# Performance work log

Measured on AMD Instinct MI355X. Metric: run time of the kernel, lower is better.

## Reference

```python
import jax, jax.numpy as jnp
import numpy as np

DIM = 2048
N_HEADS = 32
N_KV_HEADS = 8
HEAD_DIM = DIM // N_HEADS  # 64
N_REP = N_HEADS // N_KV_HEADS  # 4
B, S = 1, 2048


def _rope(t, cos, sin):
    # t: (b, s, h, head_dim); cos/sin: (s, head_dim//2)
    tr = t.reshape(*t.shape[:-1], -1, 2)
    a, b = tr[..., 0], tr[..., 1]
    c = cos[None, :, None, :]
    s_ = sin[None, :, None, :]
    ra = a * c - b * s_
    rb = a * s_ + b * c
    return jnp.stack([ra, rb], axis=-1).reshape(t.shape)


def setup_inputs() -> dict:
    key = jax.random.key(0)
    ks = jax.random.split(key, 6)
    sc = 1.0 / np.sqrt(DIM)
    x = jax.random.normal(ks[0], (B, S, DIM), dtype=jnp.float32)
    wq = jax.random.normal(ks[1], (DIM, N_HEADS * HEAD_DIM), dtype=jnp.float32) * sc
    wk = jax.random.normal(ks[2], (DIM, N_KV_HEADS * HEAD_DIM), dtype=jnp.float32) * sc
    wv = jax.random.normal(ks[3], (DIM, N_KV_HEADS * HEAD_DIM), dtype=jnp.float32) * sc
    wo = jax.random.normal(ks[4], (N_HEADS * HEAD_DIM, DIM), dtype=jnp.float32) * sc
    # rotary frequencies (theta = 500000 as in Llama3)
    inv = 1.0 / (500000.0 ** (np.arange(0, HEAD_DIM, 2, dtype=np.float32) / HEAD_DIM))
    ang = np.arange(S, dtype=np.float32)[:, None] * inv[None, :]
    freqs_cos = jnp.asarray(np.cos(ang), dtype=jnp.float32)
    freqs_sin = jnp.asarray(np.sin(ang), dtype=jnp.float32)
    # causal additive mask
    mask = jnp.triu(jnp.full((S, S), -1e9, dtype=jnp.float32), k=1)
    return {"x": x, "wq": wq, "wk": wk, "wv": wv, "wo": wo,
            "freqs_cos": freqs_cos, "freqs_sin": freqs_sin, "mask": mask,
            "start_pos": 0}


def reference(x, wq, wk, wv, wo, freqs_cos, freqs_sin, mask, start_pos):
    b, s, _ = x.shape
    xq = (x @ wq).reshape(b, s, N_HEADS, HEAD_DIM)
    xk = (x @ wk).reshape(b, s, N_KV_HEADS, HEAD_DIM)
    xv = (x @ wv).reshape(b, s, N_KV_HEADS, HEAD_DIM)
    xq = _rope(xq, freqs_cos, freqs_sin)
    xk = _rope(xk, freqs_cos, freqs_sin)
    # GQA without repeat_interleave: view queries as (b, s, kv, rep, d)
    q = xq.reshape(b, s, N_KV_HEADS, N_REP, HEAD_DIM)
    scale = 1.0 / np.sqrt(HEAD_DIM)
    # scores: (b, kv, rep, q, k)
    scores = jnp.einsum('bqkrd,bskd->bkrqs', q, xk) * scale
    scores = scores + mask[None, None, None, :, :]
    probs = jax.nn.softmax(scores.astype(jnp.float32), axis=-1).astype(x.dtype)
    out = jnp.einsum('bkrqs,bskd->bqkrd', probs, xv)
    out = out.reshape(b, s, N_HEADS * HEAD_DIM)
    return out @ wo
```

## Files before the change

### kernel.cpp

```cpp
#include <hip/hip_runtime.h>
#include <hip/hip_bf16.h>

#define DIM 2048
#define S_LEN 2048
#define N_HEADS 32
#define N_KV_HEADS 8
#define HEAD_DIM 64
#define KV_DIM (N_KV_HEADS * HEAD_DIM)
#define QKV_N (DIM + 2 * KV_DIM)
#define QSCALE 0.18033688011112042f

typedef __attribute__((ext_vector_type(8))) short bf16x8;
typedef __attribute__((ext_vector_type(4))) float f32x4;

__device__ __forceinline__ unsigned short bf16_of(float f) {
    __hip_bfloat16 h = __float2bfloat16(f);
    return *reinterpret_cast<unsigned short*>(&h);
}
__device__ __forceinline__ float f_of_bf16(unsigned short u) {
    unsigned int x = ((unsigned int)u) << 16;
    return __uint_as_float(x);
}
__device__ __forceinline__ void gl_lds16(const void* g, void* l) {
    __builtin_amdgcn_global_load_lds((const __attribute__((address_space(1))) void*)g,
                                     (__attribute__((address_space(3))) void*)l, 16, 0, 0);
}
__device__ __forceinline__ unsigned int pack2tr(float lo, float hi) {
    return __builtin_amdgcn_perm(__float_as_uint(hi), __float_as_uint(lo), 0x07060302u);
}

__global__ __launch_bounds__(256) void prep(const float* __restrict__ x,
                                            const float* __restrict__ wq,
                                            const float* __restrict__ wk,
                                            const float* __restrict__ wv,
                                            const float* __restrict__ wo,
                                            unsigned short* __restrict__ xbf,
                                            unsigned short* __restrict__ wqkvT,
                                            unsigned short* __restrict__ woT) {
    __shared__ float tile[64][65];
    const int t = threadIdx.x;
    int b = blockIdx.x;
    if (b < 4096) {
        int idx = b * 256 + t;
        float4 f = ((const float4*)x)[idx];
        ushort4 u;
        u.x = bf16_of(f.x); u.y = bf16_of(f.y); u.z = bf16_of(f.z); u.w = bf16_of(f.w);
        ((ushort4*)xbf)[idx] = u;
        return;
    }
    b -= 4096;
    const float* src;
    unsigned short* dst;
    int src_cols, bx, by;
    if (b < 1024)      { src = wq; dst = wqkvT;                                src_cols = DIM;    bx = b & 31;          by = b >> 5; }
    else if (b < 1280) { src = wk; dst = wqkvT + (size_t)DIM * DIM;            src_cols = KV_DIM; bx = (b - 1024) & 7;  by = (b - 1024) >> 3; }
    else if (b < 1536) { src = wv; dst = wqkvT + (size_t)(DIM + KV_DIM) * DIM; src_cols = KV_DIM; bx = (b - 1280) & 7;  by = (b - 1280) >> 3; }
    else               { src = wo; dst = woT;                                  src_cols = DIM;    bx = (b - 1536) & 31; by = (b - 1536) >> 5; }
    const int c0 = bx * 64, r0 = by * 64;
#pragma unroll
    for (int i = 0; i < 16; i++) {
        int idx = t + i * 256;
        int r = idx >> 6, c = idx & 63;
        tile[r][c] = src[(size_t)(r0 + r) * src_cols + c0 + c];
    }
    __syncthreads();
#pragma unroll
    for (int i = 0; i < 16; i++) {
        int idx = t + i * 256;
        int r = idx >> 6, c = idx & 63;
        dst[(size_t)(c0 + r) * DIM + r0 + c] = bf16_of(tile[c][r]);
    }
}

__global__ __launch_bounds__(256) void gemm_bt64(const unsigned short* __restrict__ A,
                                                 const unsigned short* __restrict__ Bt,
                                                 void* __restrict__ Cv,
                                                 int M, int N, int K, int c_bf16) {
    __shared__ unsigned short As[128 * 64];
    __shared__ unsigned short Bs[64 * 64];
    const int tid = threadIdx.x;
    const int wave = tid >> 6, lane = tid & 63;
    const int m16 = lane & 15, quad = lane >> 4;
    const int m0 = blockIdx.y * 128, n0 = blockIdx.x * 64;
    const int wm = (wave >> 1) * 64, wn = (wave & 1) * 32;

    const int lrow = lane >> 3;
    const int gc = (lane & 7) ^ lrow;
    const unsigned short* Ab = A + (size_t)(m0 + wave * 8 + lrow) * K + gc * 8;
    const unsigned short* Bb = Bt + (size_t)(n0 + wave * 8 + lrow) * K + gc * 8;

    f32x4 acc[4][2];
#pragma unroll
    for (int mb = 0; mb < 4; mb++)
#pragma unroll
        for (int nb = 0; nb < 2; nb++) acc[mb][nb] = (f32x4){0.f, 0.f, 0.f, 0.f};

    for (int k0 = 0; k0 < K; k0 += 64) {
#pragma unroll
        for (int g = 0; g < 4; g++)
            gl_lds16(Ab + (size_t)g * 32 * K + k0, &As[(g * 32 + wave * 8) * 64]);
#pragma unroll
        for (int g = 0; g < 2; g++)
            gl_lds16(Bb + (size_t)g * 32 * K + k0, &Bs[(g * 32 + wave * 8) * 64]);
        __syncthreads();
#pragma unroll
        for (int ks = 0; ks < 2; ks++) {
            const int ch = (ks * 4 + quad) ^ (m16 & 7);
            bf16x8 af[4], bfr[2];
#pragma unroll
            for (int mb = 0; mb < 4; mb++)
                af[mb] = *(const bf16x8*)&As[(wm + mb * 16 + m16) * 64 + ch * 8];
#pragma unroll
            for (int nb = 0; nb < 2; nb++)
                bfr[nb] = *(const bf16x8*)&Bs[(wn + nb * 16 + m16) * 64 + ch * 8];
#pragma unroll
            for (int mb = 0; mb < 4; mb++)
#pragma unroll
                for (int nb = 0; nb < 2; nb++)
                    acc[mb][nb] = __builtin_amdgcn_mfma_f32_16x16x32_bf16(af[mb], bfr[nb], acc[mb][nb], 0, 0, 0);
        }
        __syncthreads();
    }

    if (c_bf16) {
        unsigned short* C = (unsigned short*)Cv;
#pragma unroll
        for (int mb = 0; mb < 4; mb++)
#pragma unroll
            for (int nb = 0; nb < 2; nb++)
#pragma unroll
                for (int r = 0; r < 4; r++)
                    C[(size_t)(m0 + wm + mb * 16 + quad * 4 + r) * N + n0 + wn + nb * 16 + m16] =
                        bf16_of(acc[mb][nb][r]);
    } else {
        float* C = (float*)Cv;
#pragma unroll
        for (int mb = 0; mb < 4; mb++)
#pragma unroll
            for (int nb = 0; nb < 2; nb++)
#pragma unroll
                for (int r = 0; r < 4; r++)
                    C[(size_t)(m0 + wm + mb * 16 + quad * 4 + r) * N + n0 + wn + nb * 16 + m16] =
                        acc[mb][nb][r];
    }
}

__global__ __launch_bounds__(256) void rope_tv(const unsigned short* __restrict__ qkv,
                                               unsigned short* __restrict__ qbf,
                                               unsigned short* __restrict__ kbf,
                                               unsigned short* __restrict__ vbt,
                                               const float* __restrict__ fcos,
                                               const float* __restrict__ fsin) {
    __shared__ unsigned short tile[64][65];
    const int t = threadIdx.x;
    int b = blockIdx.x;
    if (b < 2560) {
        int idx = b * 256 + t;
        const int nq = S_LEN * N_HEADS * 8;
        int s, j, srcoff, dstoff;
        unsigned short* dst;
        float osc;
        if (idx < nq) {
            s = idx >> 8;
            int rem = idx & 255;
            int h = rem >> 3;
            j = rem & 7;
            srcoff = s * QKV_N + h * 64 + j * 8;
            dstoff = s * DIM + h * 64 + j * 8;
            dst = qbf;
            osc = QSCALE;
        } else {
            int t2 = idx - nq;
            s = t2 >> 6;
            int rem = t2 & 63;
            int h = rem >> 3;
            j = rem & 7;
            srcoff = s * QKV_N + DIM + h * 64 + j * 8;
            dstoff = s * KV_DIM + h * 64 + j * 8;
            dst = kbf;
            osc = 1.0f;
        }
        bf16x8 v8 = *(const bf16x8*)&qkv[srcoff];
        float4 c4 = *(const float4*)&fcos[s * 32 + j * 4];
        float4 s4 = *(const float4*)&fsin[s * 32 + j * 4];
        float cs[4] = {c4.x, c4.y, c4.z, c4.w};
        float sn[4] = {s4.x, s4.y, s4.z, s4.w};
        bf16x8 o;
#pragma unroll
        for (int p = 0; p < 4; p++) {
            float a = f_of_bf16((unsigned short)v8[2 * p]);
            float bb = f_of_bf16((unsigned short)v8[2 * p + 1]);
            o[2 * p]     = (short)bf16_of((a * cs[p] - bb * sn[p]) * osc);
            o[2 * p + 1] = (short)bf16_of((a * sn[p] + bb * cs[p]) * osc);
        }
        *(bf16x8*)&dst[dstoff] = o;
        return;
    }
    b -= 2560;
    const int d0 = (b & 7) * 64;
    const int s0 = (b >> 3) * 64;
#pragma unroll
    for (int i = 0; i < 16; i++) {
        int idx = t + i * 256;
        int r = idx >> 6, c = idx & 63;
        tile[r][c] = qkv[(size_t)(s0 + r) * QKV_N + DIM + KV_DIM + d0 + c];
    }
    __syncthreads();
#pragma unroll
    for (int i = 0; i < 16; i++) {
        int idx = t + i * 256;
        int r = idx >> 6, c = idx & 63;
        int key = s0 + c;
        int kl = key & 127;
        int kp = (kl & 0x60) | ((kl & 0x0C) << 1) | ((kl & 0x10) >> 2) | (kl & 3);
        vbt[(size_t)(d0 + r) * S_LEN + (key & ~127) + kp] = tile[c][r];
    }
}

__global__ __launch_bounds__(256) void attn_mfma5(const unsigned short* __restrict__ qb,
                                                  const unsigned short* __restrict__ kb,
                                                  const unsigned short* __restrict__ vbt,
                                                  unsigned short* __restrict__ out) {
    const int h  = blockIdx.y;
    const int bx = blockIdx.x;
    const int kh = h >> 2;
    const int tid  = threadIdx.x;
    const int wave = tid >> 6;
    const int lane = tid & 63;
    const int m16  = lane & 15;
    const int quad = lane >> 4;

    __shared__ unsigned short Ks[2][128 * 64];
    __shared__ unsigned short Vt[2][64 * 128];

    const int lrow8 = lane >> 3;
    const int kc    = (lane & 7) ^ lrow8;
    const int lrow4 = lane >> 4;
    const int vc    = (lane & 15) ^ ((wave * 4 + lrow4) & 7);

    const unsigned short* Kbase = kb + (size_t)kh * 64 + (size_t)(wave * 8 + lrow8) * KV_DIM + kc * 8;
    const unsigned short* Vbase = vbt + (size_t)(kh * 64 + wave * 4 + lrow4) * S_LEN + vc * 8;

    bf16x8 ones;
#pragma unroll
    for (int i = 0; i < 8; i++) ones[i] = (short)0x3F80;

#pragma unroll
    for (int half = 0; half < 2; half++) {
        const int qt = half ? bx : (31 - bx);
        const int q0 = qt * 64;
        const int n_iter = (qt >> 1) + 1;

        bf16x8 qa[2];
        {
            const int qrow = q0 + wave * 16 + m16;
#pragma unroll
            for (int ks = 0; ks < 2; ks++)
                qa[ks] = *(const bf16x8*)&qb[(size_t)qrow * DIM + h * 64 + ks * 32 + quad * 8];
        }

        f32x4 o_acc[4];
#pragma unroll
        for (int nb = 0; nb < 4; nb++) o_acc[nb] = (f32x4){0.f, 0.f, 0.f, 0.f};
        f32x4 l_acc = (f32x4){0.f, 0.f, 0.f, 0.f};
        float m_s = -1e30f;
        const int qrow_lane = q0 + wave * 16 + m16;
        const int orow_base = q0 + wave * 16 + quad * 4;

        if (half) __syncthreads();

#pragma unroll
        for (int g = 0; g < 4; g++) {
            gl_lds16(Kbase + (size_t)(g * 32) * KV_DIM, &Ks[0][(g * 32 + wave * 8) * 64]);
            gl_lds16(Vbase + (size_t)g * 16 * S_LEN, &Vt[0][(g * 16 + wave * 4) * 128]);
        }

        for (int kt = 0; kt < n_iter; kt++) {
            __syncthreads();
            if (kt + 1 < n_iter) {
                const int nb2 = (kt + 1) & 1;
#pragma unroll
                for (int g = 0; g < 4; g++) {
                    gl_lds16(Kbase + (size_t)((kt + 1) * 128 + g * 32) * KV_DIM,
                             &Ks[nb2][(g * 32 + wave * 8) * 64]);
                    gl_lds16(Vbase + (size_t)g * 16 * S_LEN + (kt + 1) * 128,
                             &Vt[nb2][(g * 16 + wave * 4) * 128]);
                }
            }
            const unsigned short* K_ = Ks[kt & 1];
            const unsigned short* V_ = Vt[kt & 1];

            f32x4 sc[8];
#pragma unroll
            for (int cb = 0; cb < 8; cb++) sc[cb] = (f32x4){0.f, 0.f, 0.f, 0.f};
#pragma unroll
            for (int ks = 0; ks < 2; ks++) {
                const int slot = (ks * 4 + quad) ^ (m16 & 7);
#pragma unroll
                for (int cb = 0; cb < 8; cb++) {
                    bf16x8 kf = *(const bf16x8*)&K_[(cb * 16 + m16) * 64 + slot * 8];
                    sc[cb] = __builtin_amdgcn_mfma_f32_16x16x32_bf16(kf, qa[ks], sc[cb], 0, 0, 0);
                }
            }

            if (kt == n_iter - 1) {
#pragma unroll
                for (int cb = 0; cb < 8; cb++) {
                    int key = kt * 128 + cb * 16 + quad * 4;
#pragma unroll
                    for (int r = 0; r < 4; r++)
                        if (key + r > qrow_lane) sc[cb][r] = -1e30f;
                }
            }

            float rmax = fmaxf(fmaxf(sc[0][0], sc[0][1]), fmaxf(sc[0][2], sc[0][3]));
#pragma unroll
            for (int cb = 1; cb < 8; cb++) {
                float c1 = fmaxf(fmaxf(sc[cb][0], sc[cb][1]), fmaxf(sc[cb][2], sc[cb][3]));
                rmax = fmaxf(rmax, c1);
            }
            rmax = fmaxf(rmax, __shfl_xor(rmax, 16, 64));
            rmax = fmaxf(rmax, __shfl_xor(rmax, 32, 64));

            float mnew = fmaxf(m_s, rmax);
            float alpha = __builtin_amdgcn_exp2f(m_s - mnew);
            m_s = mnew;

#pragma unroll
            for (int cb = 0; cb < 8; cb++)
#pragma unroll
                for (int r = 0; r < 4; r++)
                    sc[cb][r] = __builtin_amdgcn_exp2f(sc[cb][r] - mnew);

            unsigned int P01[8], P23[8];
#pragma unroll
            for (int cb = 0; cb < 8; cb++) {
                P01[cb] = pack2tr(sc[cb][0], sc[cb][1]);
                P23[cb] = pack2tr(sc[cb][2], sc[cb][3]);
            }

#pragma unroll
            for (int r = 0; r < 4; r++) {
                float a_r = __shfl(alpha, quad * 4 + r, 64);
#pragma unroll
                for (int nb = 0; nb < 4; nb++) o_acc[nb][r] *= a_r;
                l_acc[r] *= a_r;
            }

#pragma unroll
            for (int ks = 0; ks < 4; ks++) {
                union { unsigned int u[4]; bf16x8 v; } pa;
                pa.u[0] = P01[2 * ks];     pa.u[1] = P23[2 * ks];
                pa.u[2] = P01[2 * ks + 1]; pa.u[3] = P23[2 * ks + 1];
                const int slot = (ks * 4 + quad) ^ (m16 & 7);
#pragma unroll
                for (int nb = 0; nb < 4; nb++) {
                    bf16x8 vf = *(const bf16x8*)&V_[(nb * 16 + m16) * 128 + slot * 8];
                    o_acc[nb] = __builtin_amdgcn_mfma_f32_16x16x32_bf16(pa.v, vf, o_acc[nb], 0, 0, 0);
                }
                l_acc = __builtin_amdgcn_mfma_f32_16x16x32_bf16(pa.v, ones, l_acc, 0, 0, 0);
            }
        }

#pragma unroll
        for (int r = 0; r < 4; r++) {
            float inv_l = 1.f / l_acc[r];
#pragma unroll
            for (int nb = 0; nb < 4; nb++)
                out[(size_t)(orow_base + r) * DIM + h * 64 + nb * 16 + m16] =
                    bf16_of(o_acc[nb][r] * inv_l);
        }
    }
}

extern "C" void kernel_launch(void* const* d_in, const int* in_sizes, int n_in,
                              void* d_out, int out_size, void* d_ws, size_t ws_size,
                              hipStream_t stream) {
    const float* x    = (const float*)d_in[0];
    const float* wq   = (const float*)d_in[1];
    const float* wk   = (const float*)d_in[2];
    const float* wv   = (const float*)d_in[3];
    const float* wo   = (const float*)d_in[4];
    const float* fcos = (const float*)d_in[5];
    const float* fsin = (const float*)d_in[6];

    char* ws = (char*)d_ws;
    const size_t MB = 1024 * 1024;
    unsigned short* xbf    = (unsigned short*)(ws);
    unsigned short* wqkvT  = (unsigned short*)(ws + 8 * MB);
    unsigned short* woT    = (unsigned short*)(ws + 20 * MB);
    unsigned short* qkvbf  = (unsigned short*)(ws + 28 * MB);
    unsigned short* vbt    = (unsigned short*)(ws + 40 * MB);
    unsigned short* qbf    = (unsigned short*)(ws + 8 * MB);
    unsigned short* kbf    = (unsigned short*)(ws + 16 * MB);
    unsigned short* attnbf = (unsigned short*)(ws);

    prep<<<4096 + 2560, 256, 0, stream>>>(x, wq, wk, wv, wo, xbf, wqkvT, woT);

    gemm_bt64<<<dim3(QKV_N / 64, S_LEN / 128), 256, 0, stream>>>(xbf, wqkvT, qkvbf,
                                                                 S_LEN, QKV_N, DIM, 1);

    rope_tv<<<2560 + 256, 256, 0, stream>>>(qkvbf, qbf, kbf, vbt, fcos, fsin);

    attn_mfma5<<<dim3(16, N_HEADS), 256, 0, stream>>>(qbf, kbf, vbt, attnbf);

    gemm_bt64<<<dim3(DIM / 64, S_LEN / 128), 256, 0, stream>>>(attnbf, woT, d_out,
                                                               S_LEN, DIM, DIM, 0);
}
```

Before: 228.3 us.

## Widen QKV GEMM tile, add lazy softmax rescale, setprio and max3 in attention

The QKV projection now uses a new 128x128-tile GEMM kernel, so each block covers twice the N width and gets more operand reuse per LDS load. In the attention kernel, the online-softmax rescale of the accumulators is skipped unless the running max grows by more than 8 (log2 units), the row-max reduction uses v_max3, and the MFMA sections are wrapped in s_setprio. The prep transpose now writes two bf16 values per store. The lazy rescale lets exponentials grow up to 2^8 before rescaling, which costs a little numerical headroom, and the larger GEMM tile launches half as many blocks.

```diff
diff --git a/kernel.cpp b/kernel.cpp
--- a/kernel.cpp
+++ b/kernel.cpp
@@ -27,6 +27,11 @@
 }
 __device__ __forceinline__ unsigned int pack2tr(float lo, float hi) {
     return __builtin_amdgcn_perm(__float_as_uint(hi), __float_as_uint(lo), 0x07060302u);
+}
+__device__ __forceinline__ float max3f(float a, float b, float c) {
+    float d;
+    asm("v_max3_f32 %0, %1, %2, %3" : "=v"(d) : "v"(a), "v"(b), "v"(c));
+    return d;
 }
 
 __global__ __launch_bounds__(256) void prep(const float* __restrict__ x,
@@ -65,10 +70,13 @@
     }
     __syncthreads();
 #pragma unroll
-    for (int i = 0; i < 16; i++) {
+    for (int i = 0; i < 8; i++) {
         int idx = t + i * 256;
-        int r = idx >> 6, c = idx & 63;
-        dst[(size_t)(c0 + r) * DIM + r0 + c] = bf16_of(tile[c][r]);
+        int rr = idx >> 5, cc = (idx & 31) * 2;
+        ushort2 u2;
+        u2.x = bf16_of(tile[cc][rr]);
+        u2.y = bf16_of(tile[cc + 1][rr]);
+        *(ushort2*)&dst[(size_t)(c0 + rr) * DIM + r0 + cc] = u2;
     }
 }
 
@@ -138,6 +146,78 @@
         for (int mb = 0; mb < 4; mb++)
 #pragma unroll
             for (int nb = 0; nb < 2; nb++)
+#pragma unroll
+                for (int r = 0; r < 4; r++)
+                    C[(size_t)(m0 + wm + mb * 16 + quad * 4 + r) * N + n0 + wn + nb * 16 + m16] =
+                        acc[mb][nb][r];
+    }
+}
+
+__global__ __launch_bounds__(256) void gemm_bt128(const unsigned short* __restrict__ A,
+                                                  const unsigned short* __restrict__ Bt,
+                                                  void* __restrict__ Cv,
+                                                  int M, int N, int K, int c_bf16) {
+    __shared__ unsigned short As[128 * 64];
+    __shared__ unsigned short Bs[128 * 64];
+    const int tid = threadIdx.x;
+    const int wave = tid >> 6, lane = tid & 63;
+    const int m16 = lane & 15, quad = lane >> 4;
+    const int m0 = blockIdx.y * 128, n0 = blockIdx.x * 128;
+    const int wm = (wave >> 1) * 64, wn = (wave & 1) * 64;
+
+    const int lrow = lane >> 3;
+    const int gc = (lane & 7) ^ lrow;
+    const unsigned short* Ab = A + (size_t)(m0 + wave * 8 + lrow) * K + gc * 8;
+    const unsigned short* Bb = Bt + (size_t)(n0 + wave * 8 + lrow) * K + gc * 8;
+
+    f32x4 acc[4][4];
+#pragma unroll
+    for (int mb = 0; mb < 4; mb++)
+#pragma unroll
+        for (int nb = 0; nb < 4; nb++) acc[mb][nb] = (f32x4){0.f, 0.f, 0.f, 0.f};
+
+    for (int k0 = 0; k0 < K; k0 += 64) {
+#pragma unroll
+        for (int g = 0; g < 4; g++) {
+            gl_lds16(Ab + (size_t)g * 32 * K + k0, &As[(g * 32 + wave * 8) * 64]);
+            gl_lds16(Bb + (size_t)g * 32 * K + k0, &Bs[(g * 32 + wave * 8) * 64]);
+        }
+        __syncthreads();
+#pragma unroll
+        for (int ks = 0; ks < 2; ks++) {
+            const int ch = (ks * 4 + quad) ^ (m16 & 7);
+            bf16x8 af[4], bfr[4];
+#pragma unroll
+            for (int mb = 0; mb < 4; mb++)
+                af[mb] = *(const bf16x8*)&As[(wm + mb * 16 + m16) * 64 + ch * 8];
+#pragma unroll
+            for (int nb = 0; nb < 4; nb++)
+                bfr[nb] = *(const bf16x8*)&Bs[(wn + nb * 16 + m16) * 64 + ch * 8];
+#pragma unroll
+            for (int mb = 0; mb < 4; mb++)
+#pragma unroll
+                for (int nb = 0; nb < 4; nb++)
+                    acc[mb][nb] = __builtin_amdgcn_mfma_f32_16x16x32_bf16(af[mb], bfr[nb], acc[mb][nb], 0, 0, 0);
+        }
+        __syncthreads();
+    }
+
+    if (c_bf16) {
+        unsigned short* C = (unsigned short*)Cv;
+#pragma unroll
+        for (int mb = 0; mb < 4; mb++)
+#pragma unroll
+            for (int nb = 0; nb < 4; nb++)
+#pragma unroll
+                for (int r = 0; r < 4; r++)
+                    C[(size_t)(m0 + wm + mb * 16 + quad * 4 + r) * N + n0 + wn + nb * 16 + m16] =
+                        bf16_of(acc[mb][nb][r]);
+    } else {
+        float* C = (float*)Cv;
+#pragma unroll
+        for (int mb = 0; mb < 4; mb++)
+#pragma unroll
+            for (int nb = 0; nb < 4; nb++)
 #pragma unroll
                 for (int r = 0; r < 4; r++)
                     C[(size_t)(m0 + wm + mb * 16 + quad * 4 + r) * N + n0 + wn + nb * 16 + m16] =
@@ -217,7 +297,7 @@
     }
 }
 
-__global__ __launch_bounds__(256) void attn_mfma5(const unsigned short* __restrict__ qb,
+__global__ __launch_bounds__(256) void attn_mfma6(const unsigned short* __restrict__ qb,
                                                   const unsigned short* __restrict__ kb,
                                                   const unsigned short* __restrict__ vbt,
                                                   unsigned short* __restrict__ out) {
@@ -293,6 +373,7 @@
             f32x4 sc[8];
 #pragma unroll
             for (int cb = 0; cb < 8; cb++) sc[cb] = (f32x4){0.f, 0.f, 0.f, 0.f};
+            __builtin_amdgcn_s_setprio(1);
 #pragma unroll
             for (int ks = 0; ks < 2; ks++) {
                 const int slot = (ks * 4 + quad) ^ (m16 & 7);
@@ -302,6 +383,7 @@
                     sc[cb] = __builtin_amdgcn_mfma_f32_16x16x32_bf16(kf, qa[ks], sc[cb], 0, 0, 0);
                 }
             }
+            __builtin_amdgcn_s_setprio(0);
 
             if (kt == n_iter - 1) {
 #pragma unroll
@@ -313,24 +395,34 @@
                 }
             }
 
-            float rmax = fmaxf(fmaxf(sc[0][0], sc[0][1]), fmaxf(sc[0][2], sc[0][3]));
+            float rmax = fmaxf(sc[0][0], sc[0][1]);
+            rmax = max3f(sc[0][2], sc[0][3], rmax);
 #pragma unroll
             for (int cb = 1; cb < 8; cb++) {
-                float c1 = fmaxf(fmaxf(sc[cb][0], sc[cb][1]), fmaxf(sc[cb][2], sc[cb][3]));
-                rmax = fmaxf(rmax, c1);
+                rmax = max3f(sc[cb][0], sc[cb][1], rmax);
+                rmax = max3f(sc[cb][2], sc[cb][3], rmax);
             }
             rmax = fmaxf(rmax, __shfl_xor(rmax, 16, 64));
             rmax = fmaxf(rmax, __shfl_xor(rmax, 32, 64));
 
-            float mnew = fmaxf(m_s, rmax);
-            float alpha = __builtin_amdgcn_exp2f(m_s - mnew);
-            m_s = mnew;
+            if (!__all(rmax - m_s <= 8.0f)) {
+                float mnew = fmaxf(m_s, rmax);
+                float alpha = __builtin_amdgcn_exp2f(m_s - mnew);
+                m_s = mnew;
+#pragma unroll
+                for (int r = 0; r < 4; r++) {
+                    float a_r = __shfl(alpha, quad * 4 + r, 64);
+#pragma unroll
+                    for (int nb = 0; nb < 4; nb++) o_acc[nb][r] *= a_r;
+                    l_acc[r] *= a_r;
+                }
+            }
 
 #pragma unroll
             for (int cb = 0; cb < 8; cb++)
 #pragma unroll
                 for (int r = 0; r < 4; r++)
-                    sc[cb][r] = __builtin_amdgcn_exp2f(sc[cb][r] - mnew);
+                    sc[cb][r] = __builtin_amdgcn_exp2f(sc[cb][r] - m_s);
 
             unsigned int P01[8], P23[8];
 #pragma unroll
@@ -339,14 +431,7 @@
                 P23[cb] = pack2tr(sc[cb][2], sc[cb][3]);
             }
 
-#pragma unroll
-            for (int r = 0; r < 4; r++) {
-                float a_r = __shfl(alpha, quad * 4 + r, 64);
-#pragma unroll
-                for (int nb = 0; nb < 4; nb++) o_acc[nb][r] *= a_r;
-                l_acc[r] *= a_r;
-            }
-
+            __builtin_amdgcn_s_setprio(1);
 #pragma unroll
             for (int ks = 0; ks < 4; ks++) {
                 union { unsigned int u[4]; bf16x8 v; } pa;
@@ -360,6 +445,7 @@
                 }
                 l_acc = __builtin_amdgcn_mfma_f32_16x16x32_bf16(pa.v, ones, l_acc, 0, 0, 0);
             }
+            __builtin_amdgcn_s_setprio(0);
         }
 
 #pragma unroll
@@ -397,12 +483,12 @@
 
     prep<<<4096 + 2560, 256, 0, stream>>>(x, wq, wk, wv, wo, xbf, wqkvT, woT);
 
-    gemm_bt64<<<dim3(QKV_N / 64, S_LEN / 128), 256, 0, stream>>>(xbf, wqkvT, qkvbf,
-                                                                 S_LEN, QKV_N, DIM, 1);
+    gemm_bt128<<<dim3(QKV_N / 128, S_LEN / 128), 256, 0, stream>>>(xbf, wqkvT, qkvbf,
+                                                                   S_LEN, QKV_N, DIM, 1);
 
     rope_tv<<<2560 + 256, 256, 0, stream>>>(qkvbf, qbf, kbf, vbt, fcos, fsin);
 
-    attn_mfma5<<<dim3(16, N_HEADS), 256, 0, stream>>>(qbf, kbf, vbt, attnbf);
+    attn_mfma6<<<dim3(16, N_HEADS), 256, 0, stream>>>(qbf, kbf, vbt, attnbf);
 
     gemm_bt64<<<dim3(DIM / 64, S_LEN / 128), 256, 0, stream>>>(attnbf, woT, d_out,
                                                                S_LEN, DIM, DIM, 0);
```

Result: slower. 232.9 us (+2.0%).

## Double-buffer GEMM LDS, lazy softmax rescale, setprio and max3 in attention

Applied to the files above, without the earlier changes.

The GEMM moves to two LDS buffers so the next K tile's global-to-LDS load is issued before the current tile's MFMAs, and one barrier per iteration is dropped. In attention, the running-max rescale of the output accumulators is skipped unless some row's max grows by more than 8 (log2 domain), max reductions use v_max3, and wave priority is raised around the MFMA blocks. The weight transpose in prep now writes pairs of bf16 values at a time. The risks are higher LDS use in the GEMM, which lowers occupancy, and unnormalised exponentials up to 2^8 in attention, which stay within bf16/fp32 range.

```diff
diff --git a/kernel.cpp b/kernel.cpp
--- a/kernel.cpp
+++ b/kernel.cpp
@@ -27,6 +27,11 @@
 }
 __device__ __forceinline__ unsigned int pack2tr(float lo, float hi) {
     return __builtin_amdgcn_perm(__float_as_uint(hi), __float_as_uint(lo), 0x07060302u);
+}
+__device__ __forceinline__ float max3f(float a, float b, float c) {
+    float d;
+    asm("v_max3_f32 %0, %1, %2, %3" : "=v"(d) : "v"(a), "v"(b), "v"(c));
+    return d;
 }
 
 __global__ __launch_bounds__(256) void prep(const float* __restrict__ x,
@@ -65,10 +70,13 @@
     }
     __syncthreads();
 #pragma unroll
-    for (int i = 0; i < 16; i++) {
+    for (int i = 0; i < 8; i++) {
         int idx = t + i * 256;
-        int r = idx >> 6, c = idx & 63;
-        dst[(size_t)(c0 + r) * DIM + r0 + c] = bf16_of(tile[c][r]);
+        int rr = idx >> 5, cc = (idx & 31) * 2;
+        ushort2 u2;
+        u2.x = bf16_of(tile[cc][rr]);
+        u2.y = bf16_of(tile[cc + 1][rr]);
+        *(ushort2*)&dst[(size_t)(c0 + rr) * DIM + r0 + cc] = u2;
     }
 }
 
@@ -76,8 +84,8 @@
                                                  const unsigned short* __restrict__ Bt,
                                                  void* __restrict__ Cv,
                                                  int M, int N, int K, int c_bf16) {
-    __shared__ unsigned short As[128 * 64];
-    __shared__ unsigned short Bs[64 * 64];
+    __shared__ unsigned short As[2][128 * 64];
+    __shared__ unsigned short Bs[2][64 * 64];
     const int tid = threadIdx.x;
     const int wave = tid >> 6, lane = tid & 63;
     const int m16 = lane & 15, quad = lane >> 4;
@@ -95,31 +103,44 @@
 #pragma unroll
         for (int nb = 0; nb < 2; nb++) acc[mb][nb] = (f32x4){0.f, 0.f, 0.f, 0.f};
 
-    for (int k0 = 0; k0 < K; k0 += 64) {
-#pragma unroll
-        for (int g = 0; g < 4; g++)
-            gl_lds16(Ab + (size_t)g * 32 * K + k0, &As[(g * 32 + wave * 8) * 64]);
-#pragma unroll
-        for (int g = 0; g < 2; g++)
-            gl_lds16(Bb + (size_t)g * 32 * K + k0, &Bs[(g * 32 + wave * 8) * 64]);
+#pragma unroll
+    for (int g = 0; g < 4; g++)
+        gl_lds16(Ab + (size_t)g * 32 * K, &As[0][(g * 32 + wave * 8) * 64]);
+#pragma unroll
+    for (int g = 0; g < 2; g++)
+        gl_lds16(Bb + (size_t)g * 32 * K, &Bs[0][(g * 32 + wave * 8) * 64]);
+
+    const int nt = K >> 6;
+    for (int kt = 0; kt < nt; kt++) {
         __syncthreads();
+        if (kt + 1 < nt) {
+            const int nb2 = (kt + 1) & 1;
+            const int k0 = (kt + 1) << 6;
+#pragma unroll
+            for (int g = 0; g < 4; g++)
+                gl_lds16(Ab + (size_t)g * 32 * K + k0, &As[nb2][(g * 32 + wave * 8) * 64]);
+#pragma unroll
+            for (int g = 0; g < 2; g++)
+                gl_lds16(Bb + (size_t)g * 32 * K + k0, &Bs[nb2][(g * 32 + wave * 8) * 64]);
+        }
+        const unsigned short* A_ = As[kt & 1];
+        const unsigned short* B_ = Bs[kt & 1];
 #pragma unroll
         for (int ks = 0; ks < 2; ks++) {
             const int ch = (ks * 4 + quad) ^ (m16 & 7);
             bf16x8 af[4], bfr[2];
 #pragma unroll
             for (int mb = 0; mb < 4; mb++)
-                af[mb] = *(const bf16x8*)&As[(wm + mb * 16 + m16) * 64 + ch * 8];
+                af[mb] = *(const bf16x8*)&A_[(wm + mb * 16 + m16) * 64 + ch * 8];
 #pragma unroll
             for (int nb = 0; nb < 2; nb++)
-                bfr[nb] = *(const bf16x8*)&Bs[(wn + nb * 16 + m16) * 64 + ch * 8];
+                bfr[nb] = *(const bf16x8*)&B_[(wn + nb * 16 + m16) * 64 + ch * 8];
 #pragma unroll
             for (int mb = 0; mb < 4; mb++)
 #pragma unroll
                 for (int nb = 0; nb < 2; nb++)
                     acc[mb][nb] = __builtin_amdgcn_mfma_f32_16x16x32_bf16(af[mb], bfr[nb], acc[mb][nb], 0, 0, 0);
         }
-        __syncthreads();
     }
 
     if (c_bf16) {
@@ -217,7 +238,7 @@
     }
 }
 
-__global__ __launch_bounds__(256) void attn_mfma5(const unsigned short* __restrict__ qb,
+__global__ __launch_bounds__(256) void attn_mfma6(const unsigned short* __restrict__ qb,
                                                   const unsigned short* __restrict__ kb,
                                                   const unsigned short* __restrict__ vbt,
                                                   unsigned short* __restrict__ out) {
@@ -293,6 +314,7 @@
             f32x4 sc[8];
 #pragma unroll
             for (int cb = 0; cb < 8; cb++) sc[cb] = (f32x4){0.f, 0.f, 0.f, 0.f};
+            __builtin_amdgcn_s_setprio(1);
 #pragma unroll
             for (int ks = 0; ks < 2; ks++) {
                 const int slot = (ks * 4 + quad) ^ (m16 & 7);
@@ -302,6 +324,7 @@
                     sc[cb] = __builtin_amdgcn_mfma_f32_16x16x32_bf16(kf, qa[ks], sc[cb], 0, 0, 0);
                 }
             }
+            __builtin_amdgcn_s_setprio(0);
 
             if (kt == n_iter - 1) {
 #pragma unroll
@@ -313,24 +336,34 @@
                 }
             }
 
-            float rmax = fmaxf(fmaxf(sc[0][0], sc[0][1]), fmaxf(sc[0][2], sc[0][3]));
+            float rmax = fmaxf(sc[0][0], sc[0][1]);
+            rmax = max3f(sc[0][2], sc[0][3], rmax);
 #pragma unroll
             for (int cb = 1; cb < 8; cb++) {
-                float c1 = fmaxf(fmaxf(sc[cb][0], sc[cb][1]), fmaxf(sc[cb][2], sc[cb][3]));
-                rmax = fmaxf(rmax, c1);
+                rmax = max3f(sc[cb][0], sc[cb][1], rmax);
+                rmax = max3f(sc[cb][2], sc[cb][3], rmax);
             }
             rmax = fmaxf(rmax, __shfl_xor(rmax, 16, 64));
             rmax = fmaxf(rmax, __shfl_xor(rmax, 32, 64));
 
-            float mnew = fmaxf(m_s, rmax);
-            float alpha = __builtin_amdgcn_exp2f(m_s - mnew);
-            m_s = mnew;
+            if (!__all(rmax - m_s <= 8.0f)) {
+                float mnew = fmaxf(m_s, rmax);
+                float alpha = __builtin_amdgcn_exp2f(m_s - mnew);
+                m_s = mnew;
+#pragma unroll
+                for (int r = 0; r < 4; r++) {
+                    float a_r = __shfl(alpha, quad * 4 + r, 64);
+#pragma unroll
+                    for (int nb = 0; nb < 4; nb++) o_acc[nb][r] *= a_r;
+                    l_acc[r] *= a_r;
+                }
+            }
 
 #pragma unroll
             for (int cb = 0; cb < 8; cb++)
 #pragma unroll
                 for (int r = 0; r < 4; r++)
-                    sc[cb][r] = __builtin_amdgcn_exp2f(sc[cb][r] - mnew);
+                    sc[cb][r] = __builtin_amdgcn_exp2f(sc[cb][r] - m_s);
 
             unsigned int P01[8], P23[8];
 #pragma unroll
@@ -339,14 +372,7 @@
                 P23[cb] = pack2tr(sc[cb][2], sc[cb][3]);
             }
 
-#pragma unroll
-            for (int r = 0; r < 4; r++) {
-                float a_r = __shfl(alpha, quad * 4 + r, 64);
-#pragma unroll
-                for (int nb = 0; nb < 4; nb++) o_acc[nb][r] *= a_r;
-                l_acc[r] *= a_r;
-            }
-
+            __builtin_amdgcn_s_setprio(1);
 #pragma unroll
             for (int ks = 0; ks < 4; ks++) {
                 union { unsigned int u[4]; bf16x8 v; } pa;
@@ -360,6 +386,7 @@
                 }
                 l_acc = __builtin_amdgcn_mfma_f32_16x16x32_bf16(pa.v, ones, l_acc, 0, 0, 0);
             }
+            __builtin_amdgcn_s_setprio(0);
         }
 
 #pragma unroll
@@ -402,7 +429,7 @@
 
     rope_tv<<<2560 + 256, 256, 0, stream>>>(qkvbf, qbf, kbf, vbt, fcos, fsin);
 
-    attn_mfma5<<<dim3(16, N_HEADS), 256, 0, stream>>>(qbf, kbf, vbt, attnbf);
+    attn_mfma6<<<dim3(16, N_HEADS), 256, 0, stream>>>(qbf, kbf, vbt, attnbf);
 
     gemm_bt64<<<dim3(DIM / 64, S_LEN / 128), 256, 0, stream>>>(attnbf, woT, d_out,
                                                                S_LEN, DIM, DIM, 0);
```

Measured after the change: 221.4 us. 3.0% less time.
